# Optimization experiments

Measured on AMD Instinct MI355X. Metric: run time of the kernel, lower is better.

Reference implementation:

```python
import jax, jax.numpy as jnp
import numpy as np

B, L, V, D, H, DEPTH, M, FF, NC = 16, 1000, 8, 512, 8, 6, 256, 2048, 1
DH = D // H
SCALE = DH ** -0.5
KCONV = 33  # residual depthwise conv kernel (lucidrains default)


def layer_norm(x, s, b):
    mu = x.mean(-1, keepdims=True)
    var = ((x - mu) ** 2).mean(-1, keepdims=True)
    return (x - mu) * jax.lax.rsqrt(var + 1e-5) * s + b


def moore_penrose_pinv(x, iters=6):
    # iterative Moore-Penrose pseudoinverse (Nystromformer paper / lucidrains)
    I = jnp.eye(x.shape[-1], dtype=x.dtype)
    ax = jnp.abs(x)
    z = jnp.swapaxes(x, -1, -2) / (jnp.max(ax.sum(-1)) * jnp.max(ax.sum(-2)))
    for _ in range(iters):
        xz = x @ z
        z = 0.25 * z @ (13 * I - xz @ (15 * I - xz @ (7 * I - xz)))
    return z


def nystrom_attention(x, qkv_w, out_w, out_b, conv_k):
    b, n, d = x.shape
    pad = (M - n % M) % M  # pad on the LEFT so seq divisible by num_landmarks
    xp = jnp.pad(x, ((0, 0), (pad, 0), (0, 0)))
    N = n + pad
    q, k, v = jnp.split(xp @ qkv_w, 3, axis=-1)
    rh = lambda t: t.reshape(b, N, H, DH).transpose(0, 2, 1, 3)  # bhnd
    q, k, v = rh(q) * SCALE, rh(k), rh(v)
    l = N // M
    q_l = q.reshape(b, H, M, l, DH).mean(3)  # landmark means
    k_l = k.reshape(b, H, M, l, DH).mean(3)
    attn1 = jax.nn.softmax(jnp.einsum('bhnd,bhmd->bhnm', q, k_l), -1)
    attn2 = jax.nn.softmax(jnp.einsum('bhnd,bhmd->bhnm', q_l, k_l), -1)
    attn3 = jax.nn.softmax(jnp.einsum('bhmd,bhnd->bhmn', q_l, k), -1)
    out = (attn1 @ moore_penrose_pinv(attn2)) @ (attn3 @ v)
    # residual depthwise conv over sequence, groups=heads (Conv2d(h,h,(33,1)))
    res = jax.lax.conv_general_dilated(
        v, conv_k, (1, 1), ((KCONV // 2, KCONV // 2), (0, 0)),
        feature_group_count=H, dimension_numbers=('NCHW', 'OIHW', 'NCHW'))
    out = (out + res).transpose(0, 2, 1, 3).reshape(b, N, d)
    out = out @ out_w + out_b
    return out[:, -n:]


def setup_inputs() -> dict:
    key = jax.random.key(0)
    ks = jax.random.split(key, 9)
    s = lambda k, shape, scale=0.02: jax.random.normal(k, shape, jnp.float32) * scale
    return {
        'x': jax.random.randint(ks[0], (B, L), 0, V),
        'enc_emb': s(ks[1], (V, D), 1.0),
        'pos_emb': s(ks[2], (L, D), 1.0),
        'ln1_s': jnp.ones((DEPTH, D)), 'ln1_b': jnp.zeros((DEPTH, D)),
        'qkv_w': s(ks[3], (DEPTH, D, 3 * D)),
        'attn_out_w': s(ks[4], (DEPTH, D, D)), 'attn_out_b': jnp.zeros((DEPTH, D)),
        'conv_k': s(ks[5], (DEPTH, H, 1, KCONV, 1)),
        'ln2_s': jnp.ones((DEPTH, D)), 'ln2_b': jnp.zeros((DEPTH, D)),
        'ff_w1': s(ks[6], (DEPTH, D, FF)), 'ff_b1': jnp.zeros((DEPTH, FF)),
        'ff_w2': s(ks[7], (DEPTH, FF, D)), 'ff_b2': jnp.zeros((DEPTH, D)),
        'final_w': s(ks[8], (D * L, NC)), 'final_b': jnp.zeros((NC,)),
    }


def reference(x, enc_emb, pos_emb, ln1_s, ln1_b, qkv_w, attn_out_w, attn_out_b,
              conv_k, ln2_s, ln2_b, ff_w1, ff_b1, ff_w2, ff_b2, final_w, final_b):
    h = enc_emb[x] + pos_emb[None, :, :]  # token emb + learned posenc
    for i in range(DEPTH):
        h = h + nystrom_attention(layer_norm(h, ln1_s[i], ln1_b[i]),
                                  qkv_w[i], attn_out_w[i], attn_out_b[i], conv_k[i])
        z = layer_norm(h, ln2_s[i], ln2_b[i])
        h = h + jax.nn.gelu(z @ ff_w1[i] + ff_b1[i], approximate=False) @ ff_w2[i] + ff_b2[i]
    out = h.reshape(B, -1) @ final_w + final_b
    return out.reshape(-1)
```

## Files before the change

### kernel.cpp

```cpp
#include <hip/hip_runtime.h>
#include <hip/hip_bf16.h>
#include <math.h>

typedef unsigned short u16;
typedef unsigned int   u32;
typedef __attribute__((ext_vector_type(8))) short short8;
typedef __attribute__((ext_vector_type(4))) float f32x4;

#define L_ 1000
#define D_ 512
#define N_ 1024
#define DEPTH_ 6
#define PAD_ 24
#define SCALE_ 0.125f

__device__ inline float bf2f(u16 u){ union{u32 i; float f;} x; x.i = ((u32)u) << 16; return x.f; }
__device__ inline u16 f2bf(float f){
  union{float f; u32 i;} x; x.f = f;
  u32 r = x.i + 0x7fffu + ((x.i >> 16) & 1u);
  return (u16)(r >> 16);
}

__device__ inline void gld16(const u16* g, u16* l){
  __builtin_amdgcn_global_load_lds(
      (const __attribute__((address_space(1))) unsigned*)g,
      (__attribute__((address_space(3))) unsigned*)l, 16, 0, 0);
}

__device__ inline float blockSum256(float v, float* red){
  int t = threadIdx.x;
  #pragma unroll
  for (int o = 32; o > 0; o >>= 1) v += __shfl_down(v, o, 64);
  __syncthreads();
  if ((t & 63) == 0) red[t >> 6] = v;
  __syncthreads();
  return red[0] + red[1] + red[2] + red[3];
}
__device__ inline float blockMax256(float v, float* red){
  int t = threadIdx.x;
  #pragma unroll
  for (int o = 32; o > 0; o >>= 1) v = fmaxf(v, __shfl_down(v, o, 64));
  __syncthreads();
  if ((t & 63) == 0) red[t >> 6] = v;
  __syncthreads();
  return fmaxf(fmaxf(red[0], red[1]), fmaxf(red[2], red[3]));
}

__global__ __launch_bounds__(256) void embed_kernel(
    const int* __restrict__ x, const float* __restrict__ ee,
    const float* __restrict__ pe, float* __restrict__ h)
{
  long long i = (long long)blockIdx.x * 256 + threadIdx.x;
  int d = (int)(i & 511);
  long long bl = i >> 9;
  int l = (int)(bl % 1000);
  int tok = x[bl];
  h[i] = ee[tok * D_ + d] + pe[l * D_ + d];
}

__global__ __launch_bounds__(256) void ln_kernel(
    const float* __restrict__ in, u16* __restrict__ out,
    const float* __restrict__ sc, const float* __restrict__ bi, int pad)
{
  __shared__ float red[4];
  int r = blockIdx.x, t = threadIdx.x;
  const float* row; u16* orow;
  if (pad){
    int bb = r >> 10, n = r & 1023;
    orow = out + (long long)r * D_;
    if (n < PAD_){ orow[t] = 0; orow[t + 256] = 0; return; }
    row = in + ((long long)bb * L_ + (n - PAD_)) * D_;
  } else {
    row  = in  + (long long)r * D_;
    orow = out + (long long)r * D_;
  }
  float x0 = row[t], x1 = row[t + 256];
  float mu = blockSum256(x0 + x1, red) * (1.f / 512.f);
  float d0 = x0 - mu, d1 = x1 - mu;
  float var = blockSum256(d0 * d0 + d1 * d1, red) * (1.f / 512.f);
  float rs = rsqrtf(var + 1e-5f);
  orow[t]       = f2bf(d0 * rs * sc[t]       + bi[t]);
  orow[t + 256] = f2bf(d1 * rs * sc[t + 256] + bi[t + 256]);
}

__global__ __launch_bounds__(256) void tconv4_kernel(
    const float* __restrict__ qkvw, const float* __restrict__ ow,
    const float* __restrict__ w1, const float* __restrict__ w2,
    u16* __restrict__ qkvwT, u16* __restrict__ owT,
    u16* __restrict__ w1T, u16* __restrict__ w2T, int layer)
{
  __shared__ float tile[32][33];
  int id = blockIdx.x;
  const float* src; u16* dst; int K, N, bx, by;
  if (id < 768)      { src = qkvw + (long long)layer * 786432;  dst = qkvwT; K = 512;  N = 1536; bx = id % 48; by = id / 48; }
  else if (id < 1024){ id -= 768;  src = ow + (long long)layer * 262144;  dst = owT; K = 512;  N = 512;  bx = id % 16; by = id / 16; }
  else if (id < 2048){ id -= 1024; src = w1 + (long long)layer * 1048576; dst = w1T; K = 512;  N = 2048; bx = id % 64; by = id / 64; }
  else               { id -= 2048; src = w2 + (long long)layer * 1048576; dst = w2T; K = 2048; N = 512;  bx = id % 16; by = id / 16; }
  int kg = by << 5, ng = bx << 5;
  int t = threadIdx.x;
  int kr = t >> 3, nc = (t & 7) << 2;
  float4 v = *(const float4*)(src + (long long)(kg + kr) * N + ng + nc);
  tile[kr][nc + 0] = v.x; tile[kr][nc + 1] = v.y;
  tile[kr][nc + 2] = v.z; tile[kr][nc + 3] = v.w;
  __syncthreads();
  int nr = t >> 3, kc = (t & 7) << 2;
  ushort4 o;
  o.x = f2bf(tile[kc + 0][nr]); o.y = f2bf(tile[kc + 1][nr]);
  o.z = f2bf(tile[kc + 2][nr]); o.w = f2bf(tile[kc + 3][nr]);
  *(ushort4*)(dst + (long long)(ng + nr) * K + kg + kc) = o;
}

__global__ __launch_bounds__(256) void vtrans_kernel(
    const u16* __restrict__ qkv, u16* __restrict__ vT)
{
  __shared__ u16 tile[32][36];
  int idx = blockIdx.x;
  int bh = idx >> 6, rem = idx & 63;
  int dt = rem >> 5, nt = rem & 31;
  int b = bh >> 3, hh = bh & 7;
  int t = threadIdx.x;
  {
    int nr = t >> 3, dc = (t & 7) << 2;
    const u16* src = qkv + ((long long)b * N_ + nt * 32 + nr) * 1536 + 1024 + hh * 64 + dt * 32 + dc;
    ushort4 v = *(const ushort4*)src;
    tile[nr][dc + 0] = v.x; tile[nr][dc + 1] = v.y;
    tile[nr][dc + 2] = v.z; tile[nr][dc + 3] = v.w;
  }
  __syncthreads();
  {
    int dr = t >> 3, nc = (t & 7) << 2;
    ushort4 o;
    o.x = tile[nc + 0][dr]; o.y = tile[nc + 1][dr];
    o.z = tile[nc + 2][dr]; o.w = tile[nc + 3][dr];
    *(ushort4*)(vT + (long long)bh * 65536 + (dt * 32 + dr) * 1024 + nt * 32 + nc) = o;
  }
}

template<int OUT, int WC, int TR>
__global__ __launch_bounds__(256) void mgemm(
    const u16* __restrict__ A16, const u16* __restrict__ B16, void* __restrict__ Cv,
    u16* __restrict__ CT, const float* __restrict__ bias,
    int M, int N, int K, int lda, int ldb, int ldc, int ldct,
    long long sAb, long long sAh, long long sBb, long long sBh,
    long long sCb, long long sCh, long long sCT, int nh,
    float scale, float alpha, float beta, int flags)
{
  __shared__ __align__(16) u16 SH[18432];
  u16* As = SH;
  u16* Bs = SH + 8192;

  const int t = threadIdx.x;
  const int bz = blockIdx.z;
  const int b = bz / nh, hh = bz - b * nh;
  const int m0 = blockIdx.y << 7, n0 = blockIdx.x << 7;

  const u16* A = A16 + (long long)b * sAb + (long long)hh * sAh;
  const u16* B = B16 + (long long)b * sBb + (long long)hh * sBh;

  f32x4 acc[4][4];
  #pragma unroll
  for (int i = 0; i < 4; i++)
    #pragma unroll
    for (int j = 0; j < 4; j++) acc[i][j] = (f32x4)0.f;

  const int w = t >> 6, lane = t & 63;
  const int wm = (w >> 1) << 6, wn = (w & 1) << 6;
  const int fr = lane & 15, ko = (lane >> 4) << 3;
  const int sw = (fr & 7) << 3;

  const int sr8 = lane >> 3;
  const int sc8 = ((lane & 7) ^ sr8) << 3;
  const u16* pa[4]; const u16* pb[4]; u16* la[4]; u16* lb[4];
  #pragma unroll
  for (int q = 0; q < 4; q++){
    int ra = min(m0 + w * 32 + q * 8 + sr8, M - 1);
    int rb = min(n0 + w * 32 + q * 8 + sr8, N - 1);
    pa[q] = A + (long long)ra * lda + sc8;
    pb[q] = B + (long long)rb * ldb + sc8;
    la[q] = As + (w * 32 + q * 8) * 64 + lane * 8;
    lb[q] = Bs + (w * 32 + q * 8) * 64 + lane * 8;
  }

  for (int k0 = 0; k0 < K; k0 += 64){
    #pragma unroll
    for (int q = 0; q < 4; q++) gld16(pa[q] + k0, la[q]);
    #pragma unroll
    for (int q = 0; q < 4; q++) gld16(pb[q] + k0, lb[q]);
    __syncthreads();

    #pragma unroll
    for (int ks = 0; ks < 2; ks++){
      short8 ah[4], bhh[4];
      #pragma unroll
      for (int i = 0; i < 4; i++)
        ah[i]  = *(const short8*)(As + (wm + i*16 + fr) * 64 + (((ks << 5) + ko) ^ sw));
      #pragma unroll
      for (int j = 0; j < 4; j++)
        bhh[j] = *(const short8*)(Bs + (wn + j*16 + fr) * 64 + (((ks << 5) + ko) ^ sw));
      #pragma unroll
      for (int i = 0; i < 4; i++)
        #pragma unroll
        for (int j = 0; j < 4; j++)
          acc[i][j] = __builtin_amdgcn_mfma_f32_16x16x32_bf16(ah[i], bhh[j], acc[i][j], 0, 0, 0);
    }
    __syncthreads();
  }

  const long long coff = (long long)b * sCb + (long long)hh * sCh;
  const int quad = (lane >> 4) << 2;
  #pragma unroll
  for (int i = 0; i < 4; i++){
    #pragma unroll
    for (int j = 0; j < 4; j++){
      #pragma unroll
      for (int r = 0; r < 4; r++){
        int row = m0 + wm + i*16 + quad + r;
        int col = n0 + wn + j*16 + fr;
        if (row < M && col < N){
          float v = acc[i][j][r];
          float at = (alpha != 0.f) ? bf2f(A[(long long)row * lda + col]) : 0.f;
          float bt = (beta  != 0.f) ? bf2f(B[(long long)col * ldb + row]) : 0.f;
          v = scale * (alpha * at + beta * bt - v);
          if (flags & 4) v -= (row == col) ? 1.f : 0.f;
          if (bias) v += bias[col];
          if (flags & 2) v = 0.5f * v * (1.f + erff(v * 0.7071067811865476f));
          if constexpr (WC){
            if constexpr (OUT == 0){
              float* cp = (float*)Cv + coff + (long long)row * ldc + col;
              if (flags & 1) v += *cp;
              *cp = v;
            } else {
              u16* cp = (u16*)Cv + coff + (long long)row * ldc + col;
              if (flags & 1) v += bf2f(*cp);
              *cp = f2bf(v);
            }
          }
          if constexpr (TR)
            SH[(wn + j*16 + fr) * 144 + (wm + i*16 + quad + r)] = f2bf(v);
        }
      }
    }
  }
  if constexpr (TR){
    __syncthreads();
    const long long cofft = (long long)bz * sCT;
    #pragma unroll
    for (int c2 = 0; c2 < 8; c2++){
      int idx = c2 * 256 + t;
      int cl = idx >> 4, ms = (idx & 15) << 3;
      int gcol = n0 + cl;
      if (gcol < N && m0 + ms < M){
        uint4 val = *(const uint4*)(SH + cl * 144 + ms);
        *(uint4*)(CT + cofft + (long long)gcol * ldct + m0 + ms) = val;
      }
    }
  }
}

__global__ __launch_bounds__(256) void fattn3_kernel(
    const u16* __restrict__ ql, const u16* __restrict__ qkv,
    const u16* __restrict__ vT, u16* __restrict__ a3vT)
{
  __shared__ __align__(16) u16 Ps[4][4224];
  __shared__ __align__(16) u16 TB[4][1280];
  const int t = threadIdx.x, w = t >> 6, lane = t & 63;
  const int bh = blockIdx.y, b = bh >> 3, hh = bh & 7;
  const int m0 = blockIdx.x << 6;
  const int fr = lane & 15, ko = (lane >> 4) << 3, quad = (lane >> 4) << 2;
  const u16* qb = ql + ((long long)bh << 14) + (m0 + w * 16) * 64;
  const u16* kb = qkv + (long long)b * (N_ * 1536) + 512 + hh * 64;
  const u16* vb = vT + ((long long)bh << 16);
  u16* ps = &Ps[w][0];

  short8 aq[2];
  aq[0] = *(const short8*)(qb + fr * 64 + ko);
  aq[1] = *(const short8*)(qb + fr * 64 + 32 + ko);

  f32x4 o[4];
  #pragma unroll
  for (int j = 0; j < 4; j++) o[j] = (f32x4)0.f;
  float mrow[4] = {-1e38f, -1e38f, -1e38f, -1e38f};
  float lrow[4] = {0.f, 0.f, 0.f, 0.f};

  for (int kt = 0; kt < 4; kt++){
    f32x4 s[16];
    #pragma unroll
    for (int j = 0; j < 16; j++) s[j] = (f32x4)0.f;
    #pragma unroll
    for (int ks = 0; ks < 2; ks++)
      #pragma unroll
      for (int j = 0; j < 16; j++){
        short8 bk = *(const short8*)(kb + (long long)(kt * 256 + j * 16 + fr) * 1536 + ks * 32 + ko);
        s[j] = __builtin_amdgcn_mfma_f32_16x16x32_bf16(aq[ks], bk, s[j], 0, 0, 0);
      }
    float corr[4];
    #pragma unroll
    for (int r = 0; r < 4; r++){
      float mx = s[0][r];
      #pragma unroll
      for (int j = 1; j < 16; j++) mx = fmaxf(mx, s[j][r]);
      #pragma unroll
      for (int mk = 1; mk < 16; mk <<= 1) mx = fmaxf(mx, __shfl_xor(mx, mk, 64));
      float nm = fmaxf(mrow[r], mx);
      corr[r] = expf(mrow[r] - nm);
      mrow[r] = nm;
      float psum = 0.f;
      #pragma unroll
      for (int j = 0; j < 16; j++){
        float p = expf(s[j][r] - nm);
        psum += p;
        ps[(quad + r) * 264 + j * 16 + fr] = f2bf(p);
      }
      #pragma unroll
      for (int mk = 1; mk < 16; mk <<= 1) psum += __shfl_xor(psum, mk, 64);
      lrow[r] = lrow[r] * corr[r] + psum;
    }
    #pragma unroll
    for (int j = 0; j < 4; j++)
      #pragma unroll
      for (int r = 0; r < 4; r++) o[j][r] *= corr[r];
    #pragma unroll
    for (int ks = 0; ks < 8; ks++){
      short8 ap = *(const short8*)(ps + fr * 264 + ks * 32 + ko);
      #pragma unroll
      for (int j2 = 0; j2 < 4; j2++){
        short8 bv = *(const short8*)(vb + (j2 * 16 + fr) * 1024 + kt * 256 + ks * 32 + ko);
        o[j2] = __builtin_amdgcn_mfma_f32_16x16x32_bf16(ap, bv, o[j2], 0, 0, 0);
      }
    }
  }
  u16* tbw = &TB[w][0];
  #pragma unroll
  for (int j2 = 0; j2 < 4; j2++)
    #pragma unroll
    for (int r = 0; r < 4; r++)
      tbw[(j2 * 16 + fr) * 20 + quad + r] = f2bf(o[j2][r] / lrow[r]);
  u16* ob = a3vT + ((long long)bh << 14) + m0 + w * 16;
  #pragma unroll
  for (int q4 = 0; q4 < 4; q4++){
    ushort4 xv = *(const ushort4*)(tbw + lane * 20 + q4 * 4);
    *(ushort4*)(ob + (long long)lane * 256 + q4 * 4) = xv;
  }
}

__global__ __launch_bounds__(256) void fattn1_kernel(
    const u16* __restrict__ qkv, const u16* __restrict__ klp,
    const u16* __restrict__ wlT, u16* __restrict__ apre)
{
  __shared__ __align__(16) u16 LDS[20480];
  u16* Qs = LDS;
  u16* Ks = LDS + 4096;
  u16* Ps = LDS;
  const int t = threadIdx.x, w = t >> 6, lane = t & 63;
  const int bh = blockIdx.y, b = bh >> 3, hh = bh & 7;
  const int m0 = blockIdx.x << 6;
  const int fr = lane & 15, ko = (lane >> 4) << 3, sw = (fr & 7) << 3;
  const u16* wl = wlT + (long long)bh * 16384;

  {
    int sr = lane >> 3, sc = ((lane & 7) ^ sr) << 3;
    const u16* qbase = qkv + ((long long)b * N_ + m0) * 1536 + hh * 64 + sc;
    const u16* kbase = klp + (long long)bh * 16384 + sc;
    #pragma unroll
    for (int q = 0; q < 2; q++)
      gld16(qbase + (long long)(w*16 + q*8 + sr) * 1536, Qs + (w*16 + q*8) * 64 + lane * 8);
    #pragma unroll
    for (int q = 0; q < 8; q++)
      gld16(kbase + (w*64 + q*8 + sr) * 64, Ks + (w*64 + q*8) * 64 + lane * 8);
  }
  __syncthreads();

  f32x4 s[16];
  #pragma unroll
  for (int j = 0; j < 16; j++) s[j] = (f32x4)0.f;
  #pragma unroll
  for (int ks = 0; ks < 2; ks++){
    short8 aq = *(const short8*)(Qs + (w*16 + fr) * 64 + (((ks << 5) + ko) ^ sw));
    #pragma unroll
    for (int j = 0; j < 16; j++){
      short8 bk = *(const short8*)(Ks + (j*16 + fr) * 64 + (((ks << 5) + ko) ^ sw));
      s[j] = __builtin_amdgcn_mfma_f32_16x16x32_bf16(aq, bk, s[j], 0, 0, 0);
    }
  }
  __syncthreads();

  const int g4 = (lane >> 4) << 2, c = lane & 15;
  #pragma unroll
  for (int r = 0; r < 4; r++){
    float v[16]; float mx = -3.4e38f;
    #pragma unroll
    for (int j = 0; j < 16; j++){ v[j] = s[j][r] * SCALE_; mx = fmaxf(mx, v[j]); }
    #pragma unroll
    for (int m = 1; m < 16; m <<= 1) mx = fmaxf(mx, __shfl_xor(mx, m, 64));
    float sum = 0.f;
    #pragma unroll
    for (int j = 0; j < 16; j++){ v[j] = expf(v[j] - mx); sum += v[j]; }
    #pragma unroll
    for (int m = 1; m < 16; m <<= 1) sum += __shfl_xor(sum, m, 64);
    float inv = 1.f / sum;
    int row = w*16 + g4 + r;
    #pragma unroll
    for (int j = 0; j < 16; j++) Ps[row * 264 + j*16 + c] = f2bf(v[j] * inv);
  }

  f32x4 o[4];
  #pragma unroll
  for (int j = 0; j < 4; j++) o[j] = (f32x4)0.f;
  #pragma unroll
  for (int ks = 0; ks < 8; ks++){
    short8 ap = *(const short8*)(Ps + (w*16 + fr) * 264 + ks*32 + ko);
    #pragma unroll
    for (int j2 = 0; j2 < 4; j2++){
      short8 bw = *(const short8*)(wl + (j2*16 + fr) * 256 + ks*32 + ko);
      o[j2] = __builtin_amdgcn_mfma_f32_16x16x32_bf16(ap, bw, o[j2], 0, 0, 0);
    }
  }
  u16* ap0 = apre + (long long)b * 524288 + hh * 64;
  #pragma unroll
  for (int j2 = 0; j2 < 4; j2++)
    #pragma unroll
    for (int r = 0; r < 4; r++){
      long long n = m0 + w*16 + g4 + r;
      u16* p = ap0 + n * 512 + j2*16 + c;
      *p = f2bf(bf2f(*p) + o[j2][r]);
    }
}

__global__ __launch_bounds__(256) void fattn2_kernel(
    const u16* __restrict__ ql, const u16* __restrict__ klp, u16* __restrict__ x16)
{
  __shared__ __align__(16) u16 LDS[20480];
  u16* Qs = LDS;
  u16* Ks = LDS + 4096;
  const int t = threadIdx.x, w = t >> 6, lane = t & 63;
  const int bh = blockIdx.y;
  const int m0 = blockIdx.x << 6;
  const int fr = lane & 15, ko = (lane >> 4) << 3, sw = (fr & 7) << 3;

  {
    int sr = lane >> 3, sc = ((lane & 7) ^ sr) << 3;
    const u16* qbase = ql + (long long)bh * 16384 + m0 * 64 + sc;
    const u16* kbase = klp + (long long)bh * 16384 + sc;
    #pragma unroll
    for (int q = 0; q < 2; q++)
      gld16(qbase + (w*16 + q*8 + sr) * 64, Qs + (w*16 + q*8) * 64 + lane * 8);
    #pragma unroll
    for (int q = 0; q < 8; q++)
      gld16(kbase + (w*64 + q*8 + sr) * 64, Ks + (w*64 + q*8) * 64 + lane * 8);
  }
  __syncthreads();

  f32x4 s[16];
  #pragma unroll
  for (int j = 0; j < 16; j++) s[j] = (f32x4)0.f;
  #pragma unroll
  for (int ks = 0; ks < 2; ks++){
    short8 aq = *(const short8*)(Qs + (w*16 + fr) * 64 + (((ks << 5) + ko) ^ sw));
    #pragma unroll
    for (int j = 0; j < 16; j++){
      short8 bk = *(const short8*)(Ks + (j*16 + fr) * 64 + (((ks << 5) + ko) ^ sw));
      s[j] = __builtin_amdgcn_mfma_f32_16x16x32_bf16(aq, bk, s[j], 0, 0, 0);
    }
  }

  const int g4 = (lane >> 4) << 2, c = lane & 15;
  u16* xb = x16 + (long long)bh * 65536;
  #pragma unroll
  for (int r = 0; r < 4; r++){
    float v[16]; float mx = -3.4e38f;
    #pragma unroll
    for (int j = 0; j < 16; j++){ v[j] = s[j][r]; mx = fmaxf(mx, v[j]); }
    #pragma unroll
    for (int m = 1; m < 16; m <<= 1) mx = fmaxf(mx, __shfl_xor(mx, m, 64));
    float sum = 0.f;
    #pragma unroll
    for (int j = 0; j < 16; j++){ v[j] = expf(v[j] - mx); sum += v[j]; }
    #pragma unroll
    for (int m = 1; m < 16; m <<= 1) sum += __shfl_xor(sum, m, 64);
    float inv = 1.f / sum;
    int row = m0 + w*16 + g4 + r;
    #pragma unroll
    for (int j = 0; j < 16; j++) xb[(long long)row * 256 + j*16 + c] = f2bf(v[j] * inv);
  }
}

__global__ __launch_bounds__(256) void landmark_kernel(
    const u16* __restrict__ qkv, u16* __restrict__ ql, u16* __restrict__ kl)
{
  long long i = (long long)blockIdx.x * 256 + threadIdx.x;
  int d = (int)(i & 63);
  long long r = i >> 6;
  int m = (int)(r & 255);
  int bh = (int)(r >> 8);
  int hh = bh & 7, b = bh >> 3;
  const u16* base = qkv + ((long long)b * N_ + m * 4) * 1536 + hh * 64 + d;
  float qs = bf2f(base[0]) + bf2f(base[1536]) + bf2f(base[3072]) + bf2f(base[4608]);
  float ks = bf2f(base[512]) + bf2f(base[2048]) + bf2f(base[3584]) + bf2f(base[5120]);
  ql[i] = f2bf(qs * 0.25f * SCALE_);
  kl[i] = f2bf(ks * 0.25f);
}

__global__ void zero_kernel(float* p, int n){
  int i = blockIdx.x * 64 + threadIdx.x;
  if (i < n) p[i] = 0.f;
}
__global__ __launch_bounds__(256) void rcmax_kernel(
    const u16* __restrict__ x, float* __restrict__ scal)
{
  __shared__ float red[4];
  int bid = blockIdx.x, t = threadIdx.x;
  if (bid < 128){
    const u16* X = x + (long long)bid * 65536;
    float cs = 0.f;
    for (int m = 0; m < 256; m++) cs += fabsf(bf2f(X[m * 256 + t]));
    float cmax = blockMax256(cs, red);
    if (t == 0) atomicMax((unsigned int*)(scal + 1), __float_as_uint(cmax));
  } else {
    const u16* X = x + (long long)(bid - 128) * 65536;
    float rs = 0.f;
    for (int j = 0; j < 256; j++) rs += fabsf(bf2f(X[t * 256 + j]));
    float rmax = blockMax256(rs, red);
    if (t == 0) atomicMax((unsigned int*)(scal + 0), __float_as_uint(rmax));
  }
}
__global__ __launch_bounds__(256) void zinit_kernel(
    const u16* __restrict__ x, u16* __restrict__ z, u16* __restrict__ zt,
    const float* __restrict__ scal)
{
  float inv = 1.f / (scal[0] * scal[1]);
  long long i = (long long)blockIdx.x * 256 + threadIdx.x;
  long long bh = i >> 16;
  int ij = (int)(i & 65535);
  int ii = ij >> 8, jj = ij & 255;
  z[i]  = f2bf(bf2f(x[(bh << 16) + (jj << 8) + ii]) * inv);
  zt[i] = f2bf(bf2f(x[i]) * inv);
}

__global__ __launch_bounds__(256) void conv_kernel(
    const u16* __restrict__ qkv, const float* __restrict__ ck, u16* __restrict__ out)
{
  __shared__ u16 V[40 * 512];
  int idx = blockIdx.x;
  int b = idx >> 7, n0 = (idx & 127) << 3;
  int t = threadIdx.x;
  #pragma unroll
  for (int i = 0; i < 10; i++){
    int s = t + i * 256;
    int row = s >> 6, col8 = (s & 63) << 3;
    int n = n0 - 16 + row;
    uint4 v = make_uint4(0,0,0,0);
    if (n >= 0 && n < N_)
      v = *(const uint4*)(qkv + ((long long)b * N_ + n) * 1536 + 1024 + col8);
    *(uint4*)(V + row * 512 + col8) = v;
  }
  __syncthreads();
  int hh = t >> 5;
  float wts[33];
  #pragma unroll
  for (int k = 0; k < 33; k++) wts[k] = ck[hh * 33 + k];
  const u32* Vw = (const u32*)V;
  u32* O = (u32*)out;
  #pragma unroll 2
  for (int nn = 0; nn < 8; nn++){
    float a0 = 0.f, a1 = 0.f;
    #pragma unroll
    for (int k = 0; k < 33; k++){
      u32 pv = Vw[(nn + k) * 256 + t];
      a0 += bf2f((u16)(pv & 0xffffu)) * wts[k];
      a1 += bf2f((u16)(pv >> 16))     * wts[k];
    }
    O[((long long)b * N_ + n0 + nn) * 256 + t] = (u32)f2bf(a0) | ((u32)f2bf(a1) << 16);
  }
}

__global__ __launch_bounds__(256) void final_kernel(
    const float* __restrict__ h, const float* __restrict__ w,
    const float* __restrict__ bb, float* __restrict__ out)
{
  __shared__ float red[4];
  int b = blockIdx.x, t = threadIdx.x;
  const float* hp = h + (long long)b * (L_ * D_);
  float acc = 0.f;
  for (int i = t; i < L_ * D_; i += 256) acc += hp[i] * w[i];
  acc = blockSum256(acc, red);
  if (t == 0) out[b] = acc + bb[0];
}

template<int OUT, int WC, int TR>
static inline void mg(hipStream_t st, const void* A, const void* B, void* C, void* CT,
  const float* bias, int M, int N, int K, int lda, int ldb, int ldc, int ldct,
  long long sAb, long long sAh, long long sBb, long long sBh,
  long long sCb, long long sCh, long long sCT, int batch, int nh,
  float scale, float alpha, float beta, int flags)
{
  dim3 g((N + 127) >> 7, (M + 127) >> 7, batch);
  mgemm<OUT, WC, TR><<<g, 256, 0, st>>>((const u16*)A, (const u16*)B, C, (u16*)CT, bias,
      M, N, K, lda, ldb, ldc, ldct, sAb, sAh, sBb, sBh, sCb, sCh, sCT, nh,
      scale, alpha, beta, flags);
}

extern "C" void kernel_launch(void* const* d_in, const int* in_sizes, int n_in,
                              void* d_out, int out_size, void* d_ws, size_t ws_size,
                              hipStream_t stream)
{
  const int*   xin  = (const int*)d_in[0];
  const float* enc  = (const float*)d_in[1];
  const float* pos  = (const float*)d_in[2];
  const float* ln1s = (const float*)d_in[3];
  const float* ln1b = (const float*)d_in[4];
  const float* qkvw = (const float*)d_in[5];
  const float* ow   = (const float*)d_in[6];
  const float* ob   = (const float*)d_in[7];
  const float* ck   = (const float*)d_in[8];
  const float* ln2s = (const float*)d_in[9];
  const float* ln2b = (const float*)d_in[10];
  const float* w1   = (const float*)d_in[11];
  const float* b1   = (const float*)d_in[12];
  const float* w2   = (const float*)d_in[13];
  const float* b2   = (const float*)d_in[14];
  const float* fw   = (const float*)d_in[15];
  const float* fb   = (const float*)d_in[16];
  float* out = (float*)d_out;

  const size_t NEED = 223608896ULL;
  if (ws_size < NEED) return;

  const long long SL = 16777216;
  char* P = (char*)d_ws;
  float* h    = (float*)P; P += 32768000;
  u16*   X16  = (u16*)P;   P += 16777216;
  char*  R    = P;         P += 6 * SL;
  u16*   qkv  = (u16*)P;   P += 50331648;
  u16*   ql   = (u16*)P;   P += 4194304;
  u16*   kl   = (u16*)P;   P += 4194304;
  u16*   a3vT = (u16*)P;   P += 4194304;
  u16*   WlT  = (u16*)P;   P += 4194304;
  u16*   qkvwT= (u16*)P;   P += 1572864;
  u16*   owT  = (u16*)P;   P += 524288;
  u16*   w1T  = (u16*)P;   P += 2097152;
  u16*   w2T  = (u16*)P;   P += 2097152;
  float* scal = (float*)P; P += 64;

  u16* vT     = (u16*)(R + 4*SL);
  u16* Em     = (u16*)(R + 0*SL);
  u16* ET     = (u16*)(R + 1*SL);
  u16* Za     = (u16*)(R + 2*SL);
  u16* Zb     = (u16*)(R + 3*SL);
  u16* T1     = (u16*)(R + 4*SL);
  u16* T2     = (u16*)(R + 5*SL);
  u16* probs1 = (u16*)R;
  u16* apre   = (u16*)(R + 4*SL);
  u16* xln    = (u16*)(R + 5*SL);

  embed_kernel<<<32000, 256, 0, stream>>>(xin, enc, pos, h);

  for (int i = 0; i < DEPTH_; i++){
    tconv4_kernel<<<3072, 256, 0, stream>>>(qkvw, ow, w1, w2, qkvwT, owT, w1T, w2T, i);

    ln_kernel<<<16384, 256, 0, stream>>>(h, xln, ln1s + i * 512, ln1b + i * 512, 1);

    mg<1,1,0>(stream, xln, qkvwT, qkv, nullptr, nullptr, 16384, 1536, 512, 512, 512, 1536, 0,
              0,0, 0,0, 0,0, 0, 1, 1, -1.f, 0.f, 0.f, 0);

    landmark_kernel<<<8192, 256, 0, stream>>>(qkv, ql, kl);
    vtrans_kernel<<<8192, 256, 0, stream>>>(qkv, vT);

    fattn2_kernel<<<dim3(4, 128), 256, 0, stream>>>(ql, kl, X16);

    fattn3_kernel<<<dim3(4, 128), 256, 0, stream>>>(ql, qkv, vT, a3vT);

    zero_kernel<<<1, 64, 0, stream>>>(scal, 16);
    rcmax_kernel<<<256, 256, 0, stream>>>(X16, scal);

    zinit_kernel<<<32768, 256, 0, stream>>>(X16, Za, T1, scal);
    mg<1,1,1>(stream, X16, T1, Em, ET, nullptr, 256, 256, 256, 256, 256, 256, 256,
              65536, 0, 65536, 0, 65536, 0, 65536, 128, 1, -1.f, 0.f, 0.f, 4);
    u16 *Zc = Za, *Zn = Zb;
    for (int it = 0; it < 6; it++){
      mg<1,0,1>(stream, Em, ET, nullptr, T1, nullptr, 256, 256, 256, 256, 256, 0, 256,
                65536, 0, 65536, 0, 0, 0, 65536, 128, 1, 1.f, 5.f, 0.f, 0);
      mg<1,0,1>(stream, Em, T1, nullptr, T2, nullptr, 256, 256, 256, 256, 256, 0, 256,
                65536, 0, 65536, 0, 0, 0, 65536, 128, 1, 1.f, 9.f, -1.f, 0);
      mg<1,1,1>(stream, Zc, T2, Zn, T1, nullptr, 256, 256, 256, 256, 256, 256, 256,
                65536, 0, 65536, 0, 65536, 0, 65536, 128, 1, 0.25f, 4.f, 0.f, 0);
      if (it < 5)
        mg<1,1,1>(stream, X16, T1, Em, ET, nullptr, 256, 256, 256, 256, 256, 256, 256,
                  65536, 0, 65536, 0, 65536, 0, 65536, 128, 1, -1.f, 0.f, 0.f, 4);
      u16* tmp = Zc; Zc = Zn; Zn = tmp;
    }
    mg<1,0,1>(stream, Zc, a3vT, nullptr, WlT, nullptr, 256, 64, 256, 256, 256, 0, 256,
              65536, 0, 16384, 0, 0, 0, 16384, 128, 1, -1.f, 0.f, 0.f, 0);

    conv_kernel<<<2048, 256, 0, stream>>>(qkv, ck + i * 264, apre);

    fattn1_kernel<<<dim3(16, 128), 256, 0, stream>>>(qkv, kl, WlT, apre);

    mg<0,1,0>(stream, apre + PAD_ * 512, owT, h, nullptr, ob + i * 512,
              1000, 512, 512, 512, 512, 512, 0,
              524288, 0, 0, 0, 512000, 0, 0, 16, 1, -1.f, 0.f, 0.f, 1);

    ln_kernel<<<16000, 256, 0, stream>>>(h, xln, ln2s + i * 512, ln2b + i * 512, 0);

    for (int c = 0; c < 2; c++){
      mg<1,1,0>(stream, xln, w1T + (long long)c * 1024 * 512, probs1, nullptr,
                b1 + i * 2048 + c * 1024, 16000, 1024, 512, 512, 512, 1024, 0,
                0,0, 0,0, 0,0, 0, 1, 1, -1.f, 0.f, 0.f, 2);
      mg<0,1,0>(stream, probs1, w2T + (long long)c * 1024, h, nullptr,
                (c == 0) ? (b2 + i * 512) : nullptr,
                16000, 512, 1024, 1024, 2048, 512, 0,
                0,0, 0,0, 0,0, 0, 1, 1, -1.f, 0.f, 0.f, 1);
    }
  }

  final_kernel<<<16, 256, 0, stream>>>(h, fw, fb, out);
}
```

Measured before the change: 9.010 ms.

## Exploit symmetry of pinv iterates to drop transposed-output GEMM epilogues

Reformulates the Moore-Penrose iteration so the error matrix E = I - xz is updated algebraically (E_next = E*(polynomial)) instead of being recomputed from x and the new z each iteration. The initial scaling is folded into the GEMM epilogue through a device-side scalar. The symmetric structure lets each GEMM use the same buffer as both operands, which removes the transposed LDS writeback (TR) and the extra transposed output copies, and zinit now writes only one matrix. The risk is numerical drift, since E is propagated in bf16 rather than recomputed from x each iteration, and correctness depends on the symmetry assumptions holding.

```diff
diff --git a/kernel.cpp b/kernel.cpp
--- a/kernel.cpp
+++ b/kernel.cpp
@@ -143,7 +143,8 @@
     int M, int N, int K, int lda, int ldb, int ldc, int ldct,
     long long sAb, long long sAh, long long sBb, long long sBh,
     long long sCb, long long sCh, long long sCT, int nh,
-    float scale, float alpha, float beta, int flags)
+    float scale, float alpha, float beta, int flags,
+    const float* __restrict__ scalp)
 {
   __shared__ __align__(16) u16 SH[18432];
   u16* As = SH;
@@ -206,6 +207,9 @@
     __syncthreads();
   }
 
+  float escale = scale;
+  if (flags & 16) escale *= 1.f / (scalp[0] * scalp[1]);
+
   const long long coff = (long long)b * sCb + (long long)hh * sCh;
   const int quad = (lane >> 4) << 2;
   #pragma unroll
@@ -219,8 +223,11 @@
         if (row < M && col < N){
           float v = acc[i][j][r];
           float at = (alpha != 0.f) ? bf2f(A[(long long)row * lda + col]) : 0.f;
-          float bt = (beta  != 0.f) ? bf2f(B[(long long)col * ldb + row]) : 0.f;
-          v = scale * (alpha * at + beta * bt - v);
+          float bt = 0.f;
+          if (beta != 0.f)
+            bt = bf2f((flags & 8) ? B[(long long)row * ldb + col]
+                                  : B[(long long)col * ldb + row]);
+          v = escale * (alpha * at + beta * bt - v);
           if (flags & 4) v -= (row == col) ? 1.f : 0.f;
           if (bias) v += bias[col];
           if (flags & 2) v = 0.5f * v * (1.f + erff(v * 0.7071067811865476f));
@@ -524,16 +531,14 @@
   }
 }
 __global__ __launch_bounds__(256) void zinit_kernel(
-    const u16* __restrict__ x, u16* __restrict__ z, u16* __restrict__ zt,
-    const float* __restrict__ scal)
+    const u16* __restrict__ x, u16* __restrict__ z, const float* __restrict__ scal)
 {
   float inv = 1.f / (scal[0] * scal[1]);
   long long i = (long long)blockIdx.x * 256 + threadIdx.x;
   long long bh = i >> 16;
   int ij = (int)(i & 65535);
   int ii = ij >> 8, jj = ij & 255;
-  z[i]  = f2bf(bf2f(x[(bh << 16) + (jj << 8) + ii]) * inv);
-  zt[i] = f2bf(bf2f(x[i]) * inv);
+  z[i] = f2bf(bf2f(x[(bh << 16) + (jj << 8) + ii]) * inv);
 }
 
 __global__ __launch_bounds__(256) void conv_kernel(
@@ -591,12 +596,12 @@
   const float* bias, int M, int N, int K, int lda, int ldb, int ldc, int ldct,
   long long sAb, long long sAh, long long sBb, long long sBh,
   long long sCb, long long sCh, long long sCT, int batch, int nh,
-  float scale, float alpha, float beta, int flags)
+  float scale, float alpha, float beta, int flags, const float* scalp = nullptr)
 {
   dim3 g((N + 127) >> 7, (M + 127) >> 7, batch);
   mgemm<OUT, WC, TR><<<g, 256, 0, st>>>((const u16*)A, (const u16*)B, C, (u16*)CT, bias,
       M, N, K, lda, ldb, ldc, ldct, sAb, sAh, sBb, sBh, sCb, sCh, sCT, nh,
-      scale, alpha, beta, flags);
+      scale, alpha, beta, flags, scalp);
 }
 
 extern "C" void kernel_launch(void* const* d_in, const int* in_sizes, int n_in,
@@ -643,7 +648,7 @@
 
   u16* vT     = (u16*)(R + 4*SL);
   u16* Em     = (u16*)(R + 0*SL);
-  u16* ET     = (u16*)(R + 1*SL);
+  u16* Eb     = (u16*)(R + 1*SL);
   u16* Za     = (u16*)(R + 2*SL);
   u16* Zb     = (u16*)(R + 3*SL);
   u16* T1     = (u16*)(R + 4*SL);
@@ -672,21 +677,22 @@
     zero_kernel<<<1, 64, 0, stream>>>(scal, 16);
     rcmax_kernel<<<256, 256, 0, stream>>>(X16, scal);
 
-    zinit_kernel<<<32768, 256, 0, stream>>>(X16, Za, T1, scal);
-    mg<1,1,1>(stream, X16, T1, Em, ET, nullptr, 256, 256, 256, 256, 256, 256, 256,
-              65536, 0, 65536, 0, 65536, 0, 65536, 128, 1, -1.f, 0.f, 0.f, 4);
-    u16 *Zc = Za, *Zn = Zb;
+    zinit_kernel<<<32768, 256, 0, stream>>>(X16, Za, scal);
+    mg<1,1,0>(stream, X16, X16, Em, nullptr, nullptr, 256, 256, 256, 256, 256, 256, 0,
+              65536, 0, 65536, 0, 65536, 0, 0, 128, 1, -1.f, 0.f, 0.f, 4 | 16, scal);
+    u16 *Zc = Za, *Zn = Zb, *Ec = Em, *En = Eb;
     for (int it = 0; it < 6; it++){
-      mg<1,0,1>(stream, Em, ET, nullptr, T1, nullptr, 256, 256, 256, 256, 256, 0, 256,
-                65536, 0, 65536, 0, 0, 0, 65536, 128, 1, 1.f, 5.f, 0.f, 0);
-      mg<1,0,1>(stream, Em, T1, nullptr, T2, nullptr, 256, 256, 256, 256, 256, 0, 256,
-                65536, 0, 65536, 0, 0, 0, 65536, 128, 1, 1.f, 9.f, -1.f, 0);
-      mg<1,1,1>(stream, Zc, T2, Zn, T1, nullptr, 256, 256, 256, 256, 256, 256, 256,
-                65536, 0, 65536, 0, 65536, 0, 65536, 128, 1, 0.25f, 4.f, 0.f, 0);
+      mg<1,1,0>(stream, Ec, Ec, T1, nullptr, nullptr, 256, 256, 256, 256, 256, 256, 0,
+                65536, 0, 65536, 0, 65536, 0, 0, 128, 1, 1.f, 5.f, 0.f, 0);
+      mg<1,1,0>(stream, Ec, T1, T2, nullptr, nullptr, 256, 256, 256, 256, 256, 256, 0,
+                65536, 0, 65536, 0, 65536, 0, 0, 128, 1, 1.f, 9.f, -1.f, 8);
+      mg<1,1,0>(stream, Zc, T2, Zn, nullptr, nullptr, 256, 256, 256, 256, 256, 256, 0,
+                65536, 0, 65536, 0, 65536, 0, 0, 128, 1, 0.25f, 4.f, 0.f, 0);
       if (it < 5)
-        mg<1,1,1>(stream, X16, T1, Em, ET, nullptr, 256, 256, 256, 256, 256, 256, 256,
-                  65536, 0, 65536, 0, 65536, 0, 65536, 128, 1, -1.f, 0.f, 0.f, 4);
+        mg<1,1,0>(stream, Ec, T2, En, nullptr, nullptr, 256, 256, 256, 256, 256, 256, 0,
+                  65536, 0, 65536, 0, 65536, 0, 0, 128, 1, 0.25f, 4.f, -1.f, 8);
       u16* tmp = Zc; Zc = Zn; Zn = tmp;
+      tmp = Ec; Ec = En; En = tmp;
     }
     mg<1,0,1>(stream, Zc, a3vT, nullptr, WlT, nullptr, 256, 64, 256, 256, 256, 0, 256,
               65536, 0, 16384, 0, 0, 0, 16384, 128, 1, -1.f, 0.f, 0.f, 0);
```

Result: slower. 10.88 ms (+20.7%).
